# Optimization experiments

Hardware: AMD Instinct MI355X
Metric: run time of the kernel (lower is better)

The kernel has to match this reference:

```python
import jax, jax.numpy as jnp
import numpy as np

N = 100_000
E = 1_600_000
HID = 128
HEADS = 4
HD = HID // HEADS
EPS = 1e-5


def _ln(x, g, b):
    m = jnp.mean(x, axis=-1, keepdims=True)
    v = jnp.mean((x - m) ** 2, axis=-1, keepdims=True)
    return (x - m) * jax.lax.rsqrt(v + EPS) * g + b


def setup_inputs() -> dict:
    key = jax.random.key(0)
    ks = jax.random.split(key, 12)
    xav = lambda k, i, o: jax.random.uniform(k, (i, o), jnp.float32, -1.0, 1.0) * (0.1 * np.sqrt(6.0 / (i + o)))
    return {
        "h": jax.random.normal(ks[0], (N, HID), jnp.float32),
        "src": jax.random.randint(ks[1], (E,), 0, N, jnp.int32),
        "dst": jax.random.randint(ks[2], (E,), 0, N, jnp.int32),
        "Wq": xav(ks[3], HID, HID), "bq": jnp.zeros((HID,), jnp.float32),
        "Wk": xav(ks[4], HID, HID), "bk": jnp.zeros((HID,), jnp.float32),
        "Wv": xav(ks[5], HID, HID), "bv": jnp.zeros((HID,), jnp.float32),
        "Wo": xav(ks[6], HID, HID), "bo": jnp.zeros((HID,), jnp.float32),
        "W1": xav(ks[7], HID, 2 * HID), "b1": jnp.zeros((2 * HID,), jnp.float32),
        "W2": xav(ks[8], 2 * HID, HID), "b2": jnp.zeros((HID,), jnp.float32),
        "g1": jnp.ones((HID,), jnp.float32), "be1": jnp.zeros((HID,), jnp.float32),
        "g2": jnp.ones((HID,), jnp.float32), "be2": jnp.zeros((HID,), jnp.float32),
    }


def reference(h, src, dst, Wq, bq, Wk, bk, Wv, bv, Wo, bo, W1, b1, W2, b2, g1, be1, g2, be2):
    scale = HD ** -0.5
    h_norm = _ln(h, g1, be1)
    Q = (h_norm @ Wq + bq).reshape(N, HEADS, HD)
    K = (h_norm @ Wk + bk).reshape(N, HEADS, HD)
    V = (h_norm @ Wv + bv).reshape(N, HEADS, HD)

    # edge scores: q[dst] . k[src]  -> [E, HEADS]
    scores = jnp.sum(Q[dst] * K[src], axis=-1) * scale

    # edge softmax per destination node (segment softmax)
    smax = jax.ops.segment_max(scores, dst, num_segments=N)  # [N, HEADS]
    ex = jnp.exp(scores - smax[dst])
    denom = jax.ops.segment_sum(ex, dst, num_segments=N)
    alpha = ex / denom[dst]  # [E, HEADS]

    # weighted aggregation: sum over incoming edges of alpha * v[src]
    msgs = alpha[:, :, None] * V[src]  # [E, HEADS, HD]
    h_new = jax.ops.segment_sum(msgs, dst, num_segments=N).reshape(N, HID)

    h_attn = h_new @ Wo + bo
    h = h + h_attn  # dropout = identity (eval)
    h2 = _ln(h, g2, be2)
    ffn = jax.nn.relu(h2 @ W1 + b1) @ W2 + b2
    return h + ffn
```

## Files before the change

### kernel.cpp

```cpp
#include <hip/hip_runtime.h>
#include <math.h>

#define HIDN 128
#define EPS 1e-5f
#define ATT_SCALE 0.17677669529663687f

typedef unsigned int  u32;
typedef unsigned short u16;
typedef __attribute__((ext_vector_type(8))) short bf16x8;
typedef __attribute__((ext_vector_type(4))) float f32x4;
typedef __attribute__((ext_vector_type(2))) float f32x2;
typedef __attribute__((ext_vector_type(2))) _Float16 h16x2;

__device__ __forceinline__ u16 f2b(float x) {
    u32 u = __float_as_uint(x);
    u += 0x7FFFu + ((u >> 16) & 1u);
    return (u16)(u >> 16);
}
__device__ __forceinline__ float b2f(u16 x) { return __uint_as_float(((u32)x) << 16); }
__device__ __forceinline__ u16 f2h(float x) {
    _Float16 h = (_Float16)x;
    u16 r; __builtin_memcpy(&r, &h, 2); return r;
}
__device__ __forceinline__ h16x2 u2h(u32 a) { h16x2 r; __builtin_memcpy(&r, &a, 4); return r; }

#if __has_builtin(__builtin_amdgcn_cvt_pk_f32_fp8) && __has_builtin(__builtin_amdgcn_cvt_pk_fp8_f32)
#define HW_FP8 1
#else
#define HW_FP8 0
#endif

__device__ __forceinline__ u32 pk_fp8(float a, float b) {
#if HW_FP8
    return ((u32)__builtin_amdgcn_cvt_pk_fp8_f32(a, b, 0, false)) & 0xFFFFu;
#else
    u16 ha = f2h(a), hb = f2h(b);
    u32 b0 = (((u32)ha) + 0x80u + ((ha >> 8) & 1u)) >> 8;
    u32 b1 = (((u32)hb) + 0x80u + ((hb >> 8) & 1u)) >> 8;
    return (b0 & 0xFFu) | ((b1 & 0xFFu) << 8);
#endif
}
__device__ __forceinline__ f32x2 unpk_fp8_lo(u32 v) {
#if HW_FP8
    return __builtin_amdgcn_cvt_pk_f32_fp8(v, false);
#else
    h16x2 hh = u2h(((v & 0xFFu) << 8) | ((v & 0xFF00u) << 16));
    f32x2 r; r.x = (float)hh.x; r.y = (float)hh.y; return r;
#endif
}
__device__ __forceinline__ f32x2 unpk_fp8_hi(u32 v) {
#if HW_FP8
    return __builtin_amdgcn_cvt_pk_f32_fp8(v, true);
#else
    h16x2 hh = u2h(((v >> 16) & 0xFFu) << 8 | ((v >> 24) & 0xFFu) << 24);
    f32x2 r; r.x = (float)hh.x; r.y = (float)hh.y; return r;
#endif
}

#define MFMA(a, b, c) __builtin_amdgcn_mfma_f32_16x16x32_bf16((a), (b), (c), 0, 0, 0)

__device__ __forceinline__ int swz(int row, int kpos, int rowstride) {
    return row * rowstride + ((((kpos >> 3) ^ (row & 7)) << 3) | (kpos & 7));
}

__global__ __launch_bounds__(256) void k_pack_all(
    const float* __restrict__ Wq, const float* __restrict__ Wk, const float* __restrict__ Wv,
    const float* __restrict__ Wo, const float* __restrict__ W1, const float* __restrict__ W2,
    u16* __restrict__ out)
{
    int idx = blockIdx.x * 256 + threadIdx.x;
    const float* W; int K, N, base, local;
    if      (idx <  2048) { W = Wq; K = 128; N = 128; base = 0;     local = idx; }
    else if (idx <  4096) { W = Wk; K = 128; N = 128; base = 16384; local = idx - 2048; }
    else if (idx <  6144) { W = Wv; K = 128; N = 128; base = 32768; local = idx - 4096; }
    else if (idx <  8192) { W = Wo; K = 128; N = 128; base = 49152; local = idx - 6144; }
    else if (idx < 12288) { W = W1; K = 128; N = 256; base = 65536; local = idx - 8192; }
    else if (idx < 16384) { W = W2; K = 256; N = 128; base = 98304; local = idx - 12288; }
    else return;
    const int KC = K >> 5;
    const int l  = local & 63;
    const int tc = local >> 6;
    const int c  = tc % KC;
    const int t  = tc / KC;
    const int col = l & 15, hg = l >> 4;
    const int kbase = c * 32 + hg * 8;
    u16 v[8];
    #pragma unroll
    for (int j = 0; j < 8; ++j) v[j] = f2b(W[(size_t)(kbase + j) * N + t * 16 + col]);
    uint4 o;
    o.x = (u32)v[0] | ((u32)v[1] << 16);
    o.y = (u32)v[2] | ((u32)v[3] << 16);
    o.z = (u32)v[4] | ((u32)v[5] << 16);
    o.w = (u32)v[6] | ((u32)v[7] << 16);
    *(uint4*)&out[base + local * 8] = o;
}

__global__ __launch_bounds__(256) void k_qkv(
    const float* __restrict__ h, const float* __restrict__ g1, const float* __restrict__ be1,
    const u16* __restrict__ Bq, const u16* __restrict__ Bk, const u16* __restrict__ Bv,
    const float* __restrict__ bq, const float* __restrict__ bk, const float* __restrict__ bv,
    u16* __restrict__ Qh, u16* __restrict__ KVb, int M)
{
    __shared__ u16 smem[4][2048];
    const int wid = threadIdx.x >> 6;
    const int l   = threadIdx.x & 63;
    int slab = blockIdx.x * 4 + wid;
    const bool valid = (slab * 16) < M;
    if (!valid) slab = 0;
    const int r0  = slab * 16;
    const int col = l & 15, hg = l >> 4;
    u16* ws = smem[wid];

    float av[4][8];
    const float* hr = h + (size_t)(r0 + col) * 128 + hg * 8;
    #pragma unroll
    for (int c = 0; c < 4; ++c) {
        float4 p0 = *(const float4*)&hr[c * 32];
        float4 p1 = *(const float4*)&hr[c * 32 + 4];
        av[c][0] = p0.x; av[c][1] = p0.y; av[c][2] = p0.z; av[c][3] = p0.w;
        av[c][4] = p1.x; av[c][5] = p1.y; av[c][6] = p1.z; av[c][7] = p1.w;
    }
    float s = 0.f, q2 = 0.f;
    #pragma unroll
    for (int c = 0; c < 4; ++c)
        #pragma unroll
        for (int j = 0; j < 8; ++j) { float v = av[c][j]; s += v; q2 += v * v; }
    s  += __shfl_xor(s, 16);  s  += __shfl_xor(s, 32);
    q2 += __shfl_xor(q2, 16); q2 += __shfl_xor(q2, 32);
    float mean = s * (1.f / 128.f);
    float var  = q2 * (1.f / 128.f) - mean * mean;
    float rs   = rsqrtf(var + EPS);

    bf16x8 af[4];
    #pragma unroll
    for (int c = 0; c < 4; ++c) {
        u32 w[4];
        #pragma unroll
        for (int jj = 0; jj < 4; ++jj) {
            int k0 = c * 32 + hg * 8 + 2 * jj;
            float v0 = (av[c][2 * jj]     - mean) * rs * g1[k0]     + be1[k0];
            float v1 = (av[c][2 * jj + 1] - mean) * rs * g1[k0 + 1] + be1[k0 + 1];
            w[jj] = (u32)f2b(v0) | ((u32)f2b(v1) << 16);
        }
        uint4 uu = make_uint4(w[0], w[1], w[2], w[3]);
        af[c] = *(bf16x8*)&uu;
    }

    #pragma unroll
    for (int t = 0; t < 8; ++t) {
        float bb = bq[t * 16 + col];
        f32x4 c = {bb, bb, bb, bb};
        const u16* bp = Bq + t * 2048 + l * 8;
        c = MFMA(af[0], *(const bf16x8*)(bp),        c);
        c = MFMA(af[1], *(const bf16x8*)(bp + 512),  c);
        c = MFMA(af[2], *(const bf16x8*)(bp + 1024), c);
        c = MFMA(af[3], *(const bf16x8*)(bp + 1536), c);
        #pragma unroll
        for (int r = 0; r < 4; ++r)
            ws[swz(hg * 4 + r, t * 16 + col, 128)] = f2h(c[r]);
    }
    __syncthreads();
    if (valid) {
        #pragma unroll
        for (int i = 0; i < 4; ++i) {
            int row = i * 4 + (l >> 4);
            int cg  = l & 15;
            bf16x8 vv = *(const bf16x8*)&ws[swz(row, cg * 8, 128)];
            *(bf16x8*)&Qh[(size_t)(r0 + row) * 128 + cg * 8] = vv;
        }
    }
    __syncthreads();

    #pragma unroll
    for (int t = 0; t < 8; ++t) {
        float bb = bk[t * 16 + col];
        f32x4 c = {bb, bb, bb, bb};
        const u16* bp = Bk + t * 2048 + l * 8;
        c = MFMA(af[0], *(const bf16x8*)(bp),        c);
        c = MFMA(af[1], *(const bf16x8*)(bp + 512),  c);
        c = MFMA(af[2], *(const bf16x8*)(bp + 1024), c);
        c = MFMA(af[3], *(const bf16x8*)(bp + 1536), c);
        int cc = t * 16 + col;
        int ki = ((cc >> 3) << 3) | ((cc & 7) >> 1);
        #pragma unroll
        for (int r = 0; r < 4; ++r) {
            float other = __shfl_xor(c[r], 1);
            if ((col & 1) == 0)
                ws[swz(hg * 4 + r, ki, 128)] = (u16)pk_fp8(c[r], other);
        }
    }
    #pragma unroll
    for (int t = 0; t < 8; ++t) {
        float bb = bv[t * 16 + col];
        f32x4 c = {bb, bb, bb, bb};
        const u16* bp = Bv + t * 2048 + l * 8;
        c = MFMA(af[0], *(const bf16x8*)(bp),        c);
        c = MFMA(af[1], *(const bf16x8*)(bp + 512),  c);
        c = MFMA(af[2], *(const bf16x8*)(bp + 1024), c);
        c = MFMA(af[3], *(const bf16x8*)(bp + 1536), c);
        int cc = t * 16 + col;
        int vi = (((cc >> 3) << 3) | ((cc & 7) >> 1)) + 4;
        #pragma unroll
        for (int r = 0; r < 4; ++r) {
            float other = __shfl_xor(c[r], 1);
            if ((col & 1) == 0)
                ws[swz(hg * 4 + r, vi, 128)] = (u16)pk_fp8(c[r], other);
        }
    }
    __syncthreads();
    if (valid) {
        #pragma unroll
        for (int i = 0; i < 4; ++i) {
            int row = i * 4 + (l >> 4);
            int cg  = l & 15;
            bf16x8 vv = *(const bf16x8*)&ws[swz(row, cg * 8, 128)];
            *(bf16x8*)&KVb[(size_t)(r0 + row) * 128 + cg * 8] = vv;
        }
    }
}

#define BSH 8
#define CHUNK 4096

__global__ __launch_bounds__(256) void k_bcount(
    const int* __restrict__ dst, int* __restrict__ bcnt, int e)
{
    __shared__ int hist[512];
    const int tid = threadIdx.x;
    hist[tid] = 0; hist[tid + 256] = 0;
    __syncthreads();
    const int i0 = blockIdx.x * CHUNK;
    #pragma unroll
    for (int t = 0; t < CHUNK / 256; ++t) {
        int i = i0 + t * 256 + tid;
        if (i < e) atomicAdd(&hist[dst[i] >> BSH], 1);
    }
    __syncthreads();
    for (int j = tid; j < 512; j += 256) {
        int c = hist[j];
        if (c) atomicAdd(&bcnt[j], c);
    }
}

__global__ __launch_bounds__(512) void k_bscan(
    const int* __restrict__ bcnt, int* __restrict__ bbase, int* __restrict__ bcur, int nbuck)
{
    __shared__ int ts[512];
    const int tid = threadIdx.x;
    int v = (tid < nbuck) ? bcnt[tid] : 0;
    ts[tid] = v;
    __syncthreads();
    for (int off = 1; off < 512; off <<= 1) {
        int x = (tid >= off) ? ts[tid - off] : 0;
        __syncthreads();
        ts[tid] += x;
        __syncthreads();
    }
    int ex = ts[tid] - v;
    if (tid <= nbuck) bbase[tid] = ex;
    if (tid < nbuck)  bcur[tid]  = ex;
}

__global__ __launch_bounds__(256) void k_bscatter(
    const int* __restrict__ src, const int* __restrict__ dst,
    int* __restrict__ bcur, int2* __restrict__ ebuf, int e)
{
    __shared__ int hist[512];
    __shared__ int lbase[512];
    __shared__ int lrun[512];
    const int tid = threadIdx.x;
    hist[tid] = 0; hist[tid + 256] = 0;
    __syncthreads();
    const int i0 = blockIdx.x * CHUNK;
    #pragma unroll
    for (int t = 0; t < CHUNK / 256; ++t) {
        int i = i0 + t * 256 + tid;
        if (i < e) atomicAdd(&hist[dst[i] >> BSH], 1);
    }
    __syncthreads();
    for (int j = tid; j < 512; j += 256) {
        int c = hist[j];
        lrun[j] = 0;
        if (c) lbase[j] = atomicAdd(&bcur[j], c);
    }
    __syncthreads();
    #pragma unroll
    for (int t = 0; t < CHUNK / 256; ++t) {
        int i = i0 + t * 256 + tid;
        if (i < e) {
            int d = dst[i];
            int b = d >> BSH;
            int r = atomicAdd(&lrun[b], 1);
            ebuf[lbase[b] + r] = make_int2(src[i], d);
        }
    }
}

__global__ __launch_bounds__(256) void k_bbuild(
    const int2* __restrict__ ebuf, const int* __restrict__ bbase,
    int* __restrict__ cnt, int* __restrict__ offs, int* __restrict__ csrc, int n)
{
    __shared__ int ncnt[256];
    __shared__ int ts[256];
    __shared__ int nrun[256];
    const int tid = threadIdx.x;
    const int b = blockIdx.x;
    const int node0 = b << BSH;
    const int nn = min(256, n - node0);
    const int s = bbase[b];
    const int epb = bbase[b + 1] - s;

    ncnt[tid] = 0;
    __syncthreads();
    for (int i = tid; i < epb; i += 256)
        atomicAdd(&ncnt[ebuf[s + i].y & 255], 1);
    __syncthreads();
    int v = ncnt[tid];
    ts[tid] = v;
    __syncthreads();
    for (int off = 1; off < 256; off <<= 1) {
        int x = (tid >= off) ? ts[tid - off] : 0;
        __syncthreads();
        ts[tid] += x;
        __syncthreads();
    }
    int ex = ts[tid] - v;
    if (tid < nn) { cnt[node0 + tid] = v; offs[node0 + tid] = s + ex; }
    nrun[tid] = 0;
    __syncthreads();
    ncnt[tid] = ex;
    __syncthreads();
    for (int i = tid; i < epb; i += 256) {
        int2 p = ebuf[s + i];
        int d = p.y & 255;
        int r = atomicAdd(&nrun[d], 1);
        csrc[s + ncnt[d] + r] = p.x;
    }
}

__global__ __launch_bounds__(256) void k_edge(
    const u16* __restrict__ Qh, const u16* __restrict__ KVb,
    const int* __restrict__ offs, const int* __restrict__ cnt, const int* __restrict__ csrc,
    u16* __restrict__ hnew, int n)
{
    const int wid  = threadIdx.x >> 6;
    const int l    = threadIdx.x & 63;
    const int node = blockIdx.x * 4 + wid;
    if (node >= n) return;
    const int start = offs[node];
    const int deg   = cnt[node];
    const int w    = l & 15;
    const int slot = l >> 4;

    const uint4 q = *(const uint4*)&Qh[(size_t)node * 128 + w * 8];
    float qf[8];
    { h16x2 t;
      t = u2h(q.x); qf[0] = (float)t.x; qf[1] = (float)t.y;
      t = u2h(q.y); qf[2] = (float)t.x; qf[3] = (float)t.y;
      t = u2h(q.z); qf[4] = (float)t.x; qf[5] = (float)t.y;
      t = u2h(q.w); qf[6] = (float)t.x; qf[7] = (float)t.y; }

    float of[8] = {0, 0, 0, 0, 0, 0, 0, 0};
    float denom = 0.f;

    for (int base = 0; base < deg; base += 64) {
        int m = deg - base; if (m > 64) m = 64;
        int myidx = 0;
        if (l < m) myidx = csrc[start + base + l];
        for (int j = 0; j < m; j += 4) {
            int eloc = j + slot;
            int s = __shfl(myidx, eloc & 63);
            const uint4 kv = *(const uint4*)&KVb[(size_t)s * 128 + w * 8];
            f32x2 k01 = unpk_fp8_lo(kv.x), k23 = unpk_fp8_hi(kv.x);
            f32x2 k45 = unpk_fp8_lo(kv.y), k67 = unpk_fp8_hi(kv.y);
            float p;
            p = qf[0] * k01.x;
            p = fmaf(qf[1], k01.y, p);
            p = fmaf(qf[2], k23.x, p);
            p = fmaf(qf[3], k23.y, p);
            p = fmaf(qf[4], k45.x, p);
            p = fmaf(qf[5], k45.y, p);
            p = fmaf(qf[6], k67.x, p);
            p = fmaf(qf[7], k67.y, p);
            p += __shfl_xor(p, 1);
            p += __shfl_xor(p, 2);
            float al = __expf(p * ATT_SCALE);
            al = (eloc < m) ? al : 0.f;
            denom += al;
            f32x2 v01 = unpk_fp8_lo(kv.z), v23 = unpk_fp8_hi(kv.z);
            f32x2 v45 = unpk_fp8_lo(kv.w), v67 = unpk_fp8_hi(kv.w);
            of[0] = fmaf(al, v01.x, of[0]);
            of[1] = fmaf(al, v01.y, of[1]);
            of[2] = fmaf(al, v23.x, of[2]);
            of[3] = fmaf(al, v23.y, of[3]);
            of[4] = fmaf(al, v45.x, of[4]);
            of[5] = fmaf(al, v45.y, of[5]);
            of[6] = fmaf(al, v67.x, of[6]);
            of[7] = fmaf(al, v67.y, of[7]);
        }
    }

    #pragma unroll
    for (int msk = 16; msk <= 32; msk <<= 1) {
        #pragma unroll
        for (int i = 0; i < 8; ++i) of[i] += __shfl_xor(of[i], msk);
        denom += __shfl_xor(denom, msk);
    }
    float inv = (deg > 0) ? (1.f / denom) : 0.f;
    if (slot == 0) {
        u32 wrd[4];
        #pragma unroll
        for (int i = 0; i < 4; ++i)
            wrd[i] = (u32)f2b(of[2 * i] * inv) | ((u32)f2b(of[2 * i + 1] * inv) << 16);
        uint4 uu = make_uint4(wrd[0], wrd[1], wrd[2], wrd[3]);
        *(uint4*)&hnew[(size_t)node * 128 + w * 8] = uu;
    }
}

__global__ __launch_bounds__(256) void k_attnout(
    const u16* __restrict__ hnew, const u16* __restrict__ Bo, const float* __restrict__ bo,
    const float* __restrict__ h, const float* __restrict__ g2, const float* __restrict__ be2,
    float* __restrict__ h1, u16* __restrict__ h2, int M)
{
    const int slab = blockIdx.x * 4 + (threadIdx.x >> 6);
    const int l = threadIdx.x & 63;
    const int r0 = slab * 16;
    if (r0 >= M) return;
    const int col = l & 15, hg = l >> 4;
    const u16* ar = hnew + (size_t)(r0 + col) * 128 + hg * 8;
    bf16x8 a0 = *(const bf16x8*)(ar);
    bf16x8 a1 = *(const bf16x8*)(ar + 32);
    bf16x8 a2 = *(const bf16x8*)(ar + 64);
    bf16x8 a3 = *(const bf16x8*)(ar + 96);
    f32x4 acc[8];
    #pragma unroll
    for (int t = 0; t < 8; ++t) {
        float bb = bo[t * 16 + col];
        f32x4 c = {bb, bb, bb, bb};
        const u16* bp = Bo + t * 2048 + l * 8;
        c = MFMA(a0, *(const bf16x8*)(bp),        c);
        c = MFMA(a1, *(const bf16x8*)(bp + 512),  c);
        c = MFMA(a2, *(const bf16x8*)(bp + 1024), c);
        c = MFMA(a3, *(const bf16x8*)(bp + 1536), c);
        acc[t] = c;
    }
    float s[4] = {0, 0, 0, 0}, s2[4] = {0, 0, 0, 0};
    #pragma unroll
    for (int t = 0; t < 8; ++t) {
        #pragma unroll
        for (int r = 0; r < 4; ++r) {
            float x = acc[t][r] + h[(size_t)(r0 + hg * 4 + r) * 128 + t * 16 + col];
            acc[t][r] = x;
            s[r] += x; s2[r] += x * x;
        }
    }
    float mean[4], rs[4];
    #pragma unroll
    for (int r = 0; r < 4; ++r) {
        float a = s[r], b = s2[r];
        a += __shfl_xor(a, 1); b += __shfl_xor(b, 1);
        a += __shfl_xor(a, 2); b += __shfl_xor(b, 2);
        a += __shfl_xor(a, 4); b += __shfl_xor(b, 4);
        a += __shfl_xor(a, 8); b += __shfl_xor(b, 8);
        mean[r] = a * (1.f / 128.f);
        float var = b * (1.f / 128.f) - mean[r] * mean[r];
        rs[r] = rsqrtf(var + EPS);
    }
    #pragma unroll
    for (int t = 0; t < 8; ++t) {
        float g  = g2[t * 16 + col];
        float be = be2[t * 16 + col];
        #pragma unroll
        for (int r = 0; r < 4; ++r) {
            size_t idx = (size_t)(r0 + hg * 4 + r) * 128 + t * 16 + col;
            float x = acc[t][r];
            h1[idx] = x;
            h2[idx] = f2b((x - mean[r]) * rs[r] * g + be);
        }
    }
}

__global__ __launch_bounds__(256) void k_ffn1(
    const u16* __restrict__ h2, const u16* __restrict__ B1, const float* __restrict__ b1,
    u16* __restrict__ tb, int M)
{
    const int slab = blockIdx.x * 4 + (threadIdx.x >> 6);
    const int l = threadIdx.x & 63;
    const int r0 = slab * 16;
    if (r0 >= M) return;
    const int col = l & 15, hg = l >> 4;
    const u16* ar = h2 + (size_t)(r0 + col) * 128 + hg * 8;
    bf16x8 a0 = *(const bf16x8*)(ar);
    bf16x8 a1 = *(const bf16x8*)(ar + 32);
    bf16x8 a2 = *(const bf16x8*)(ar + 64);
    bf16x8 a3 = *(const bf16x8*)(ar + 96);
    #pragma unroll
    for (int t = 0; t < 16; ++t) {
        float bb = b1[t * 16 + col];
        f32x4 c = {bb, bb, bb, bb};
        const u16* bp = B1 + t * 2048 + l * 8;
        c = MFMA(a0, *(const bf16x8*)(bp),        c);
        c = MFMA(a1, *(const bf16x8*)(bp + 512),  c);
        c = MFMA(a2, *(const bf16x8*)(bp + 1024), c);
        c = MFMA(a3, *(const bf16x8*)(bp + 1536), c);
        #pragma unroll
        for (int r = 0; r < 4; ++r)
            tb[(size_t)(r0 + hg * 4 + r) * 256 + t * 16 + col] = f2b(fmaxf(c[r], 0.f));
    }
}

__global__ __launch_bounds__(256) void k_ffn2(
    const u16* __restrict__ tb, const u16* __restrict__ B2, const float* __restrict__ b2,
    const float* __restrict__ h1, float* __restrict__ out, int M)
{
    const int slab = blockIdx.x * 4 + (threadIdx.x >> 6);
    const int l = threadIdx.x & 63;
    const int r0 = slab * 16;
    if (r0 >= M) return;
    const int col = l & 15, hg = l >> 4;
    const u16* ar = tb + (size_t)(r0 + col) * 256 + hg * 8;
    bf16x8 a[8];
    #pragma unroll
    for (int i = 0; i < 8; ++i) a[i] = *(const bf16x8*)(ar + i * 32);
    #pragma unroll
    for (int t = 0; t < 8; ++t) {
        float bb = b2[t * 16 + col];
        f32x4 c = {bb, bb, bb, bb};
        const u16* bp = B2 + t * 4096 + l * 8;
        #pragma unroll
        for (int kc = 0; kc < 8; ++kc)
            c = MFMA(a[kc], *(const bf16x8*)(bp + kc * 512), c);
        #pragma unroll
        for (int r = 0; r < 4; ++r) {
            size_t idx = (size_t)(r0 + hg * 4 + r) * 128 + t * 16 + col;
            out[idx] = c[r] + h1[idx];
        }
    }
}

extern "C" void kernel_launch(void* const* d_in, const int* in_sizes, int n_in,
                              void* d_out, int out_size, void* d_ws, size_t ws_size,
                              hipStream_t stream)
{
    const float* h   = (const float*)d_in[0];
    const int*   src = (const int*)  d_in[1];
    const int*   dst = (const int*)  d_in[2];
    const float* Wq  = (const float*)d_in[3];
    const float* bq  = (const float*)d_in[4];
    const float* Wk  = (const float*)d_in[5];
    const float* bk  = (const float*)d_in[6];
    const float* Wv  = (const float*)d_in[7];
    const float* bv  = (const float*)d_in[8];
    const float* Wo  = (const float*)d_in[9];
    const float* bo  = (const float*)d_in[10];
    const float* W1  = (const float*)d_in[11];
    const float* b1  = (const float*)d_in[12];
    const float* W2  = (const float*)d_in[13];
    const float* b2  = (const float*)d_in[14];
    const float* g1  = (const float*)d_in[15];
    const float* be1 = (const float*)d_in[16];
    const float* g2  = (const float*)d_in[17];
    const float* be2 = (const float*)d_in[18];

    const int n = in_sizes[0] / HIDN;
    const int e = in_sizes[1];
    float* out = (float*)d_out;

    const int nbuck = (n + 255) >> BSH;

    char* p = (char*)d_ws;
    int* csrc  = (int*)p;              p += (size_t)e * 4;
    int* cnt   = (int*)p;              p += (size_t)n * 4;
    int* offs  = (int*)p;              p += (size_t)n * 4;
    int* bcnt  = (int*)p;              p += 512 * 4;
    int* bbase = (int*)p;              p += 512 * 4;
    int* bcur  = (int*)p;              p += 512 * 4;
    u16* wpack = (u16*)p;              p += 131072 * 2;
    u16* KVb  = (u16*)p;               p += (size_t)n * 128 * 2;
    u16* Qh   = (u16*)p;               p += (size_t)n * 128 * 2;
    u16* hnew = (u16*)p;               p += (size_t)n * 128 * 2;
    float* h1 = (float*)p;             p += (size_t)n * 128 * 4;
    u16* tb   = (u16*)p;               p += (size_t)n * 256 * 2;
    u16* h2 = Qh;
    int2* ebuf = (int2*)h1;

    u16* Wq_p = wpack;
    u16* Wk_p = wpack + 16384;
    u16* Wv_p = wpack + 32768;
    u16* Wo_p = wpack + 49152;
    u16* W1_p = wpack + 65536;
    u16* W2_p = wpack + 98304;

    const int nslab = (n + 15) / 16;
    const int gemm_blocks = (nslab + 3) / 4;
    const int echunks = (e + CHUNK - 1) / CHUNK;

    hipMemsetAsync(bcnt, 0, 512 * sizeof(int), stream);

    k_bcount  <<<echunks, 256, 0, stream>>>(dst, bcnt, e);
    k_bscan   <<<1, 512, 0, stream>>>(bcnt, bbase, bcur, nbuck);
    k_bscatter<<<echunks, 256, 0, stream>>>(src, dst, bcur, ebuf, e);
    k_bbuild  <<<nbuck, 256, 0, stream>>>(ebuf, bbase, cnt, offs, csrc, n);

    k_pack_all<<<64, 256, 0, stream>>>(Wq, Wk, Wv, Wo, W1, W2, wpack);

    k_qkv <<<gemm_blocks, 256, 0, stream>>>(h, g1, be1, Wq_p, Wk_p, Wv_p,
                                            bq, bk, bv, Qh, KVb, n);

    k_edge<<<(n + 3) / 4, 256, 0, stream>>>(Qh, KVb, offs, cnt, csrc, hnew, n);

    k_attnout<<<gemm_blocks, 256, 0, stream>>>(hnew, Wo_p, bo, h, g2, be2, h1, h2, n);

    k_ffn1<<<gemm_blocks, 256, 0, stream>>>(h2, W1_p, b1, tb, n);

    k_ffn2<<<gemm_blocks, 256, 0, stream>>>(tb, W2_p, b2, h1, out, n);
}
```

Measured before the change: 408.5 us.

## Fuse FFN GEMMs through shared memory and pack edge buffer into 32-bit words

Merges the two FFN kernels into one. The ReLU hidden activations of each 16-row slab stay in per-wave swizzled shared memory instead of going through a global bf16 buffer, which removes the write and re-read of an N×256 intermediate and one launch. Separately, the bucket scatter now packs each edge's src index and the low 8 bits of dst into a single u32, halving ebuf traffic. This assumes node ids fit in 24 bits, and it adds 32KB of LDS per block, which may reduce occupancy.

```diff
diff --git a/kernel.cpp b/kernel.cpp
--- a/kernel.cpp
+++ b/kernel.cpp
@@ -263,7 +263,7 @@
 
 __global__ __launch_bounds__(256) void k_bscatter(
     const int* __restrict__ src, const int* __restrict__ dst,
-    int* __restrict__ bcur, int2* __restrict__ ebuf, int e)
+    int* __restrict__ bcur, u32* __restrict__ ebuf, int e)
 {
     __shared__ int hist[512];
     __shared__ int lbase[512];
@@ -291,13 +291,13 @@
             int d = dst[i];
             int b = d >> BSH;
             int r = atomicAdd(&lrun[b], 1);
-            ebuf[lbase[b] + r] = make_int2(src[i], d);
+            ebuf[lbase[b] + r] = (u32)src[i] | ((u32)(d & 255) << 24);
         }
     }
 }
 
 __global__ __launch_bounds__(256) void k_bbuild(
-    const int2* __restrict__ ebuf, const int* __restrict__ bbase,
+    const u32* __restrict__ ebuf, const int* __restrict__ bbase,
     int* __restrict__ cnt, int* __restrict__ offs, int* __restrict__ csrc, int n)
 {
     __shared__ int ncnt[256];
@@ -313,7 +313,7 @@
     ncnt[tid] = 0;
     __syncthreads();
     for (int i = tid; i < epb; i += 256)
-        atomicAdd(&ncnt[ebuf[s + i].y & 255], 1);
+        atomicAdd(&ncnt[ebuf[s + i] >> 24], 1);
     __syncthreads();
     int v = ncnt[tid];
     ts[tid] = v;
@@ -331,10 +331,10 @@
     ncnt[tid] = ex;
     __syncthreads();
     for (int i = tid; i < epb; i += 256) {
-        int2 p = ebuf[s + i];
-        int d = p.y & 255;
+        u32 p = ebuf[s + i];
+        int d = p >> 24;
         int r = atomicAdd(&nrun[d], 1);
-        csrc[s + ncnt[d] + r] = p.x;
+        csrc[s + ncnt[d] + r] = (int)(p & 0xFFFFFFu);
     }
 }
 
@@ -480,48 +480,45 @@
     }
 }
 
-__global__ __launch_bounds__(256) void k_ffn1(
+__global__ __launch_bounds__(256) void k_ffn(
     const u16* __restrict__ h2, const u16* __restrict__ B1, const float* __restrict__ b1,
-    u16* __restrict__ tb, int M)
-{
-    const int slab = blockIdx.x * 4 + (threadIdx.x >> 6);
-    const int l = threadIdx.x & 63;
-    const int r0 = slab * 16;
-    if (r0 >= M) return;
+    const u16* __restrict__ B2, const float* __restrict__ b2,
+    const float* __restrict__ h1, float* __restrict__ out, int M)
+{
+    __shared__ u16 smem[4][4096];
+    const int wid = threadIdx.x >> 6;
+    const int l   = threadIdx.x & 63;
+    int slab = blockIdx.x * 4 + wid;
+    const bool valid = (slab * 16) < M;
+    if (!valid) slab = 0;
+    const int r0  = slab * 16;
     const int col = l & 15, hg = l >> 4;
+    u16* ws = smem[wid];
+
     const u16* ar = h2 + (size_t)(r0 + col) * 128 + hg * 8;
-    bf16x8 a0 = *(const bf16x8*)(ar);
-    bf16x8 a1 = *(const bf16x8*)(ar + 32);
-    bf16x8 a2 = *(const bf16x8*)(ar + 64);
-    bf16x8 a3 = *(const bf16x8*)(ar + 96);
+    bf16x8 f1a = *(const bf16x8*)(ar);
+    bf16x8 f1b = *(const bf16x8*)(ar + 32);
+    bf16x8 f1c = *(const bf16x8*)(ar + 64);
+    bf16x8 f1d = *(const bf16x8*)(ar + 96);
+
     #pragma unroll
     for (int t = 0; t < 16; ++t) {
         float bb = b1[t * 16 + col];
         f32x4 c = {bb, bb, bb, bb};
         const u16* bp = B1 + t * 2048 + l * 8;
-        c = MFMA(a0, *(const bf16x8*)(bp),        c);
-        c = MFMA(a1, *(const bf16x8*)(bp + 512),  c);
-        c = MFMA(a2, *(const bf16x8*)(bp + 1024), c);
-        c = MFMA(a3, *(const bf16x8*)(bp + 1536), c);
+        c = MFMA(f1a, *(const bf16x8*)(bp),        c);
+        c = MFMA(f1b, *(const bf16x8*)(bp + 512),  c);
+        c = MFMA(f1c, *(const bf16x8*)(bp + 1024), c);
+        c = MFMA(f1d, *(const bf16x8*)(bp + 1536), c);
         #pragma unroll
         for (int r = 0; r < 4; ++r)
-            tb[(size_t)(r0 + hg * 4 + r) * 256 + t * 16 + col] = f2b(fmaxf(c[r], 0.f));
-    }
-}
-
-__global__ __launch_bounds__(256) void k_ffn2(
-    const u16* __restrict__ tb, const u16* __restrict__ B2, const float* __restrict__ b2,
-    const float* __restrict__ h1, float* __restrict__ out, int M)
-{
-    const int slab = blockIdx.x * 4 + (threadIdx.x >> 6);
-    const int l = threadIdx.x & 63;
-    const int r0 = slab * 16;
-    if (r0 >= M) return;
-    const int col = l & 15, hg = l >> 4;
-    const u16* ar = tb + (size_t)(r0 + col) * 256 + hg * 8;
-    bf16x8 a[8];
-    #pragma unroll
-    for (int i = 0; i < 8; ++i) a[i] = *(const bf16x8*)(ar + i * 32);
+            ws[swz(hg * 4 + r, t * 16 + col, 256)] = f2b(fmaxf(c[r], 0.f));
+    }
+    __syncthreads();
+    bf16x8 f2[8];
+    #pragma unroll
+    for (int i = 0; i < 8; ++i)
+        f2[i] = *(const bf16x8*)&ws[swz(col, i * 32 + hg * 8, 256)];
     #pragma unroll
     for (int t = 0; t < 8; ++t) {
         float bb = b2[t * 16 + col];
@@ -529,11 +526,13 @@
         const u16* bp = B2 + t * 4096 + l * 8;
         #pragma unroll
         for (int kc = 0; kc < 8; ++kc)
-            c = MFMA(a[kc], *(const bf16x8*)(bp + kc * 512), c);
-        #pragma unroll
-        for (int r = 0; r < 4; ++r) {
-            size_t idx = (size_t)(r0 + hg * 4 + r) * 128 + t * 16 + col;
-            out[idx] = c[r] + h1[idx];
+            c = MFMA(f2[kc], *(const bf16x8*)(bp + kc * 512), c);
+        if (valid) {
+            #pragma unroll
+            for (int r = 0; r < 4; ++r) {
+                size_t idx = (size_t)(r0 + hg * 4 + r) * 128 + t * 16 + col;
+                out[idx] = c[r] + h1[idx];
+            }
         }
     }
 }
@@ -580,9 +579,8 @@
     u16* Qh   = (u16*)p;               p += (size_t)n * 128 * 2;
     u16* hnew = (u16*)p;               p += (size_t)n * 128 * 2;
     float* h1 = (float*)p;             p += (size_t)n * 128 * 4;
-    u16* tb   = (u16*)p;               p += (size_t)n * 256 * 2;
     u16* h2 = Qh;
-    int2* ebuf = (int2*)h1;
+    u32* ebuf = (u32*)h1;
 
     u16* Wq_p = wpack;
     u16* Wk_p = wpack + 16384;
@@ -611,7 +609,5 @@
 
     k_attnout<<<gemm_blocks, 256, 0, stream>>>(hnew, Wo_p, bo, h, g2, be2, h1, h2, n);
 
-    k_ffn1<<<gemm_blocks, 256, 0, stream>>>(h2, W1_p, b1, tb, n);
-
-    k_ffn2<<<gemm_blocks, 256, 0, stream>>>(tb, W2_p, b2, h1, out, n);
-}
+    k_ffn <<<gemm_blocks, 256, 0, stream>>>(h2, W1_p, b1, W2_p, b2, h1, out, n);
+}
```

Result: faster. 395.2 us (-3.3%).
